# Performance work log

Measured on AMD Instinct MI355X. Metric: run time of the kernel, lower is better.

Reference implementation:

```python
import jax, jax.numpy as jnp
import numpy as np
from jax import lax

ALPHA = 1.0
BETA = 2.0
NUM_ANTS = 16384
NUM_NODES = 512
BATCH = 4096


def setup_inputs() -> dict:
    key = jax.random.key(0)
    k1, k2, k3 = jax.random.split(key, 3)
    x = jax.random.normal(k1, (BATCH, NUM_NODES), dtype=jnp.float32)
    # matches nn.Parameter(torch.ones(N,N)*0.1)
    pheromone_trails = jnp.ones((NUM_NODES, NUM_NODES), dtype=jnp.float32) * 0.1
    # matches nn.Parameter(torch.rand(N,N)*0.1)
    heuristic_info = jax.random.uniform(k2, (NUM_NODES, NUM_NODES), dtype=jnp.float32) * 0.1
    # matches register_buffer('ant_positions', randint(0, N, (num_ants,)))
    ant_positions = jax.random.randint(k3, (NUM_ANTS,), 0, NUM_NODES, dtype=jnp.int32)
    return {"x": x, "pheromone_trails": pheromone_trails,
            "heuristic_info": heuristic_info, "ant_positions": ant_positions}


def reference(x, pheromone_trails, heuristic_info, ant_positions):
    A, N = NUM_ANTS, NUM_NODES
    ant_ids = jnp.arange(A)

    # NOTE: the torch code's select_next_node always reads the row of the ant's
    # *initial* position (self.ant_positions is never updated inside forward),
    # so the unmasked scores are constant per ant. We replicate that faithfully.
    base = (pheromone_trails[ant_positions] ** ALPHA) * \
           (heuristic_info[ant_positions] ** BETA)          # [A, N]

    visited0 = jnp.zeros((A, N), dtype=bool).at[ant_ids, ant_positions].set(True)
    plen0 = jnp.zeros((A,), dtype=jnp.float32)

    def step(carry, _):
        key, visited, current, plen = carry
        key, sub = jax.random.split(key)
        # torch sets masked entries to 0 (NOT -inf) before softmax; replicate.
        logits = jnp.where(visited, 0.0, base)               # [A, N]
        # categorical == multinomial(softmax(logits), 1), vectorized over ants
        nxt = jax.random.categorical(sub, logits, axis=-1)   # [A] int
        plen = plen + heuristic_info[current, nxt]
        visited = visited.at[ant_ids, nxt].set(True)
        return (key, visited, nxt, plen), nxt

    carry0 = (jax.random.key(42), visited0, ant_positions.astype(jnp.int32), plen0)
    (_, _, _, path_lengths), sampled = lax.scan(step, carry0, None, length=N - 1)

    # full paths: [A, N] = start node followed by N-1 sampled nodes
    paths = jnp.concatenate([ant_positions[:, None].astype(sampled.dtype),
                             sampled.T], axis=1)
    # sequential 'if path_length < best' with strict < keeps the FIRST minimum,
    # which is exactly jnp.argmin
    best_idx = jnp.argmin(path_lengths)
    best_path = paths[best_idx].astype(jnp.float32)          # [N]
    return jnp.broadcast_to(best_path[None, :], (x.shape[0], N))
```

## Files before the change

### kernel.cpp

```cpp
#include <hip/hip_runtime.h>
#include <cstdint>
#include <cstddef>

#define A_NUM_ANTS   16384
#define N_NODES      512
#define N_STEPS      511
#define N_BATCH      4096

constexpr uint32_t rotl32(uint32_t x, int r) { return (x << r) | (x >> (32 - r)); }

constexpr void tf2x32(uint32_t k0, uint32_t k1, uint32_t x0, uint32_t x1,
                      uint32_t& o0, uint32_t& o1) {
  const uint32_t k2 = k0 ^ k1 ^ 0x1BD11BDAu;
  x0 += k0; x1 += k1;
  x0 += x1; x1 = rotl32(x1, 13); x1 ^= x0;
  x0 += x1; x1 = rotl32(x1, 15); x1 ^= x0;
  x0 += x1; x1 = rotl32(x1, 26); x1 ^= x0;
  x0 += x1; x1 = rotl32(x1,  6); x1 ^= x0;
  x0 += k1; x1 += k2 + 1u;
  x0 += x1; x1 = rotl32(x1, 17); x1 ^= x0;
  x0 += x1; x1 = rotl32(x1, 29); x1 ^= x0;
  x0 += x1; x1 = rotl32(x1, 16); x1 ^= x0;
  x0 += x1; x1 = rotl32(x1, 24); x1 ^= x0;
  x0 += k2; x1 += k0 + 2u;
  x0 += x1; x1 = rotl32(x1, 13); x1 ^= x0;
  x0 += x1; x1 = rotl32(x1, 15); x1 ^= x0;
  x0 += x1; x1 = rotl32(x1, 26); x1 ^= x0;
  x0 += x1; x1 = rotl32(x1,  6); x1 ^= x0;
  x0 += k0; x1 += k1 + 3u;
  x0 += x1; x1 = rotl32(x1, 17); x1 ^= x0;
  x0 += x1; x1 = rotl32(x1, 29); x1 ^= x0;
  x0 += x1; x1 = rotl32(x1, 16); x1 ^= x0;
  x0 += x1; x1 = rotl32(x1, 24); x1 ^= x0;
  x0 += k1; x1 += k2 + 4u;
  x0 += x1; x1 = rotl32(x1, 13); x1 ^= x0;
  x0 += x1; x1 = rotl32(x1, 15); x1 ^= x0;
  x0 += x1; x1 = rotl32(x1, 26); x1 ^= x0;
  x0 += x1; x1 = rotl32(x1,  6); x1 ^= x0;
  x0 += k2; x1 += k0 + 5u;
  o0 = x0; o1 = x1;
}

struct Subkeys { uint32_t k0[N_STEPS]; uint32_t k1[N_STEPS]; };

constexpr Subkeys make_subkeys() {
  Subkeys s{};
  uint32_t c0 = 0u, c1 = 42u;
  for (int t = 0; t < N_STEPS; ++t) {
    uint32_t n0 = 0, n1 = 0, s0 = 0, s1 = 0;
    tf2x32(c0, c1, 0u, 0u, n0, n1);
    tf2x32(c0, c1, 0u, 1u, s0, s1);
    s.k0[t] = s0; s.k1[t] = s1;
    c0 = n0; c1 = n1;
  }
  return s;
}

namespace { constexpr Subkeys H_SUBKEYS = make_subkeys(); }
__device__ __constant__ Subkeys SUBKEYS = H_SUBKEYS;

#define NEG_LN2   (-0.69314718056f)

template <bool WRITE_PATH>
__device__ __forceinline__ void simulate_ant(
    int a, int lane,
    const float* __restrict__ pher,
    const float* __restrict__ heur,
    int pos,
    float* __restrict__ plen_out,
    float* __restrict__ path_out)
{
  float lm[8];
  {
    const float* hrow = heur + (size_t)pos * N_NODES;
    const float* prow = pher + (size_t)pos * N_NODES;
#pragma unroll
    for (int q = 0; q < 8; ++q) {
      const int n = lane * 8 + q;
      const float hv = hrow[n];
      const float base = prow[n] * (hv * hv);
      lm[q] = NEG_LN2 * expf(-base);
      if (n == pos) lm[q] = NEG_LN2;
    }
  }

  int baddr[6];
#pragma unroll
  for (int r = 0; r < 6; ++r) baddr[r] = ((lane ^ (1 << r)) << 2);

  int   cur  = pos;
  float plen = 0.0f;
  if (WRITE_PATH && lane == 0) path_out[0] = (float)pos;

  const uint32_t ctr_base = (uint32_t)(a * N_NODES + lane * 8);
  const int lane8 = lane * 8;

  for (int t = 0; t < N_STEPS; ++t) {
    const uint32_t k0 = SUBKEYS.k0[t];
    const uint32_t k1 = SUBKEYS.k1[t];

    float s[8];
#pragma unroll
    for (int q = 0; q < 8; ++q) {
      uint32_t o0, o1;
      tf2x32(k0, k1, 0u, ctr_base + (uint32_t)q, o0, o1);
      const uint32_t bits = o0 ^ o1;
      const float f = __uint_as_float((bits >> 9) | 0x3f800000u) - 1.0f;
      s[q] = __log2f(f) * lm[q];
    }
    float smin = s[0];
#pragma unroll
    for (int q = 1; q < 8; ++q) smin = fminf(smin, s[q]);
#pragma unroll
    for (int r = 0; r < 6; ++r) {
      const int other = __builtin_amdgcn_ds_bpermute(baddr[r], __float_as_int(smin));
      smin = fminf(smin, __int_as_float(other));
    }
    int fq = 8;
#pragma unroll
    for (int q = 7; q >= 0; --q) if (s[q] == smin) fq = q;
    const unsigned long long mask = __ballot(fq < 8);
    const int winlane = __builtin_ctzll(mask);
    const int bn = __shfl(fq, winlane, 64) + winlane * 8;

#pragma unroll
    for (int q = 0; q < 8; ++q)
      if (lane8 + q == bn) lm[q] = NEG_LN2;

    plen += heur[(size_t)cur * N_NODES + bn];
    cur = bn;
    if (WRITE_PATH && lane == 0) path_out[t + 1] = (float)bn;
  }

  if (!WRITE_PATH && lane == 0) plen_out[a] = plen;
}

__global__ __launch_bounds__(256, 6) void aco_sim_kernel(
    const float* __restrict__ pher, const float* __restrict__ heur,
    const int* __restrict__ pos0, float* __restrict__ plen_out, int num_ants)
{
  const int a = (int)((blockIdx.x * blockDim.x + threadIdx.x) >> 6);
  const int lane = threadIdx.x & 63;
  if (a >= num_ants) return;
  simulate_ant<false>(a, lane, pher, heur, pos0[a], plen_out, nullptr);
}

__global__ void aco_argmin_kernel(const float* __restrict__ plen,
                                  int* __restrict__ best, int num_ants) {
  const int tid = threadIdx.x;
  float bv = 3.4e38f;
  int   bi = 0;
  bool  have = false;
  for (int i = tid; i < num_ants; i += 256) {
    const float v = plen[i];
    if (!have || v < bv) { bv = v; bi = i; have = true; }
  }
#pragma unroll
  for (int off = 32; off >= 1; off >>= 1) {
    const float vo = __shfl_xor(bv, off, 64);
    const int   io = __shfl_xor(bi, off, 64);
    if (vo < bv || (vo == bv && io < bi)) { bv = vo; bi = io; }
  }
  __shared__ float sv[4];
  __shared__ int   si[4];
  const int w = tid >> 6;
  if ((tid & 63) == 0) { sv[w] = bv; si[w] = bi; }
  __syncthreads();
  if (tid == 0) {
    for (int j = 1; j < 4; ++j)
      if (sv[j] < bv || (sv[j] == bv && si[j] < bi)) { bv = sv[j]; bi = si[j]; }
    bi = bi < 0 ? 0 : (bi >= num_ants ? num_ants - 1 : bi);
    *best = bi;
  }
}

__global__ void aco_resim_kernel(const float* __restrict__ pher,
                                 const float* __restrict__ heur,
                                 const int* __restrict__ pos0,
                                 const int* __restrict__ best,
                                 float* __restrict__ path_out, int num_ants) {
  const int lane = threadIdx.x & 63;
  int a = *best;
  a = a < 0 ? 0 : (a >= num_ants ? num_ants - 1 : a);
  simulate_ant<true>(a, lane, pher, heur, pos0[a], nullptr, path_out);
}

__global__ void aco_bcast_kernel(float* __restrict__ out, int total4) {
  const int j = (int)(blockIdx.x * blockDim.x + threadIdx.x);
  if (j >= total4) return;
  const int row  = 1 + (j >> 7);
  const int col4 = j & 127;
  const float4 v = reinterpret_cast<const float4*>(out)[col4];
  reinterpret_cast<float4*>(out)[row * 128 + col4] = v;
}

extern "C" void kernel_launch(void* const* d_in, const int* in_sizes, int n_in,
                              void* d_out, int out_size, void* d_ws, size_t ws_size,
                              hipStream_t stream) {
  const float* pher = (const float*)d_in[1];
  const float* heur = (const float*)d_in[2];
  const int*   pos  = (const int*)d_in[3];
  float* out = (float*)d_out;
  const int num_ants = in_sizes[3];

  float* plen = out;
  int*   best = (int*)(out + A_NUM_ANTS);

  const int sim_blocks = (num_ants * 64 + 255) / 256;
  aco_sim_kernel<<<dim3(sim_blocks), dim3(256), 0, stream>>>(
      pher, heur, pos, plen, num_ants);
  aco_argmin_kernel<<<dim3(1), dim3(256), 0, stream>>>(plen, best, num_ants);
  aco_resim_kernel<<<dim3(1), dim3(64), 0, stream>>>(
      pher, heur, pos, best, out, num_ants);
  const int total4 = (out_size - N_NODES) / 4;
  aco_bcast_kernel<<<dim3((total4 + 255) / 256), dim3(256), 0, stream>>>(
      out, total4);
}
```

Before: 8.845 ms.

## Add fast-path winner selection by max uniform bits with bounded-ratio threshold

Each step now takes the wavefront-wide maximum of the raw uniform mantissa bits and computes a threshold. The threshold comes from the global ratio of max to min exp(-base) weights, and any candidate below it provably cannot win. When exactly one candidate passes, that node is chosen directly, skipping the per-element log2, multiply and float min-reduction. Visited state moves from overwriting lm to a bitmask. The exact path still runs when several candidates pass, and the result depends on the threshold margins being conservative enough to keep sampling bit-exact.

```diff
diff --git a/kernel.cpp b/kernel.cpp
--- a/kernel.cpp
+++ b/kernel.cpp
@@ -70,62 +70,106 @@
     float* __restrict__ plen_out,
     float* __restrict__ path_out)
 {
-  float lm[8];
+  float    lm[8];
+  uint32_t visited = 0;
+  float    ebmin, ebmax;
   {
     const float* hrow = heur + (size_t)pos * N_NODES;
     const float* prow = pher + (size_t)pos * N_NODES;
+    ebmin = 1.0f; ebmax = 1.0f;
 #pragma unroll
     for (int q = 0; q < 8; ++q) {
       const int n = lane * 8 + q;
       const float hv = hrow[n];
       const float base = prow[n] * (hv * hv);
-      lm[q] = NEG_LN2 * expf(-base);
-      if (n == pos) lm[q] = NEG_LN2;
+      const float eb = expf(-base);
+      lm[q] = NEG_LN2 * eb;
+      ebmin = fminf(ebmin, eb);
+      ebmax = fmaxf(ebmax, eb);
+      if (n == pos) visited |= (1u << q);
     }
   }
 
   int baddr[6];
 #pragma unroll
   for (int r = 0; r < 6; ++r) baddr[r] = ((lane ^ (1 << r)) << 2);
+
+#pragma unroll
+  for (int r = 0; r < 6; ++r) {
+    ebmin = fminf(ebmin, __int_as_float(
+        __builtin_amdgcn_ds_bpermute(baddr[r], __float_as_int(ebmin))));
+    ebmax = fmaxf(ebmax, __int_as_float(
+        __builtin_amdgcn_ds_bpermute(baddr[r], __float_as_int(ebmax))));
+  }
+  const float allow = (ebmax / ebmin) * (1.0f + 2e-4f);
 
   int   cur  = pos;
   float plen = 0.0f;
   if (WRITE_PATH && lane == 0) path_out[0] = (float)pos;
 
   const uint32_t ctr_base = (uint32_t)(a * N_NODES + lane * 8);
-  const int lane8 = lane * 8;
 
   for (int t = 0; t < N_STEPS; ++t) {
     const uint32_t k0 = SUBKEYS.k0[t];
     const uint32_t k1 = SUBKEYS.k1[t];
 
-    float s[8];
+    uint32_t m[8];
 #pragma unroll
     for (int q = 0; q < 8; ++q) {
       uint32_t o0, o1;
       tf2x32(k0, k1, 0u, ctr_base + (uint32_t)q, o0, o1);
-      const uint32_t bits = o0 ^ o1;
-      const float f = __uint_as_float((bits >> 9) | 0x3f800000u) - 1.0f;
-      s[q] = __log2f(f) * lm[q];
-    }
-    float smin = s[0];
-#pragma unroll
-    for (int q = 1; q < 8; ++q) smin = fminf(smin, s[q]);
+      m[q] = (o0 ^ o1) >> 9;
+    }
+    uint32_t mmax = m[0];
+#pragma unroll
+    for (int q = 1; q < 8; ++q) mmax = mmax > m[q] ? mmax : m[q];
 #pragma unroll
     for (int r = 0; r < 6; ++r) {
-      const int other = __builtin_amdgcn_ds_bpermute(baddr[r], __float_as_int(smin));
-      smin = fminf(smin, __int_as_float(other));
-    }
-    int fq = 8;
-#pragma unroll
-    for (int q = 7; q >= 0; --q) if (s[q] == smin) fq = q;
-    const unsigned long long mask = __ballot(fq < 8);
-    const int winlane = __builtin_ctzll(mask);
-    const int bn = __shfl(fq, winlane, 64) + winlane * 8;
-
-#pragma unroll
-    for (int q = 0; q < 8; ++q)
-      if (lane8 + q == bn) lm[q] = NEG_LN2;
+      const uint32_t o = (uint32_t)__builtin_amdgcn_ds_bpermute(baddr[r], (int)mmax);
+      mmax = mmax > o ? mmax : o;
+    }
+    const float L    = 23.0f - __log2f((float)mmax);
+    const float uthr = __builtin_amdgcn_exp2f(-L * allow);
+    const uint32_t mthr = (uint32_t)(uthr * 8388608.0f * (1.0f - 1e-4f));
+
+    unsigned long long b[8];
+    int tot = 0;
+#pragma unroll
+    for (int q = 0; q < 8; ++q) {
+      b[q] = __ballot(m[q] >= mthr);
+      tot += __popcll(b[q]);
+    }
+
+    int bn;
+    if (tot == 1) {
+      bn = 0;
+#pragma unroll
+      for (int q = 0; q < 8; ++q)
+        if (b[q]) bn = (int)__builtin_ctzll(b[q]) * 8 + q;
+    } else {
+      float s[8];
+#pragma unroll
+      for (int q = 0; q < 8; ++q) {
+        const float f  = __uint_as_float(m[q] | 0x3f800000u) - 1.0f;
+        const float le = ((visited >> q) & 1u) ? NEG_LN2 : lm[q];
+        s[q] = __log2f(f) * le;
+      }
+      float smin = s[0];
+#pragma unroll
+      for (int q = 1; q < 8; ++q) smin = fminf(smin, s[q]);
+#pragma unroll
+      for (int r = 0; r < 6; ++r)
+        smin = fminf(smin, __int_as_float(
+            __builtin_amdgcn_ds_bpermute(baddr[r], __float_as_int(smin))));
+      int fq = 8;
+#pragma unroll
+      for (int q = 7; q >= 0; --q) if (s[q] == smin) fq = q;
+      const unsigned long long mask = __ballot(fq < 8);
+      const int winlane = __builtin_ctzll(mask);
+      bn = __shfl(fq, winlane, 64) + winlane * 8;
+    }
+
+    if ((bn >> 3) == lane) visited |= (1u << (bn & 7));
 
     plen += heur[(size_t)cur * N_NODES + bn];
     cur = bn;
```

New measurement: 8.506 ms. -3.8%, faster.
